# Kernel tuning notes

Hardware: AMD Instinct MI355X
Metric: run time of the kernel (lower is better)

The kernel has to match this reference:

```python
import jax, jax.numpy as jnp
import numpy as np

B, S, D, H = 4, 256, 128, 8
HD = D // H          # head_dim = 16
DD = D // 2          # desc dim = 64 (required: 2*DD == H*HD for edge_type='normal')
T = S + 1            # new_seq (CLS + variables)
NEG_INF = -1e9


def setup_inputs() -> dict:
    key = jax.random.key(0)
    ks = jax.random.split(key, 8)
    p = lambda k, shape: jax.random.normal(k, shape, dtype=jnp.float32) * 0.05
    return {
        "desc_embeddings": jax.random.normal(ks[0], (B, S, DD), dtype=jnp.float32),
        "name_value_embeddings": jax.random.normal(ks[1], (B, T, D), dtype=jnp.float32),
        "Wq": p(ks[2], (D, D)), "bq": jnp.zeros((D,), jnp.float32),
        "Wk": p(ks[3], (D, D)), "bk": jnp.zeros((D,), jnp.float32),
        "Wv": p(ks[4], (D, D)), "bv": jnp.zeros((D,), jnp.float32),
        "aw": p(ks[5], (3 * HD,)),               # attn_proj weight (Linear(3*head_dim, 1))
        "ab": jnp.zeros((), jnp.float32),         # attn_proj bias
    }


def reference(desc_embeddings, name_value_embeddings, Wq, bq, Wk, bk, Wv, bv, aw, ab):
    # Projections -> [B, H, T, HD]
    def proj(W, b):
        y = name_value_embeddings @ W.T + b
        return y.reshape(B, T, H, HD).transpose(0, 2, 1, 3)
    q = proj(Wq, bq)
    k = proj(Wk, bk)
    v = proj(Wv, bv)

    # Structural adjacency: Var-Var without self loops, CLS->Var on, Var->CLS off.
    var_adj = 1.0 - jnp.eye(S, dtype=jnp.float32)          # no_self_loop=True
    adj = jnp.zeros((T, T), jnp.float32)
    adj = adj.at[1:, 1:].set(var_adj).at[0, 1:].set(1.0)   # [T, T], same for all batches

    # Edge attributes: e[b,i,j] = [desc_i, desc_j] on Var-Var block; [desc, desc] on CLS row/col.
    de = desc_embeddings                                    # [B, S, DD]
    edge = jnp.zeros((B, T, T, 2 * DD), jnp.float32)
    edge = edge.at[:, 1:, 1:, :DD].set(de[:, :, None, :])
    edge = edge.at[:, 1:, 1:, DD:].set(de[:, None, :, :])
    cls_e = jnp.concatenate([de, de], axis=-1)              # [B, S, 2*DD]
    edge = edge.at[:, 0, 1:, :].set(cls_e).at[:, 1:, 0, :].set(cls_e)
    eh = edge.reshape(B, T, T, H, HD)                       # per-head edge features

    # attn_proj(cat([q_i, k_j, e_ij])) decomposes linearly (gat_v1: no nonlinearity before):
    # score = q_i.aq + k_j.ak + (adj * e_ij).ae + bias   (edge masked by adjacency pre-linear)
    aq, ak, ae = aw[:HD], aw[HD:2 * HD], aw[2 * HD:]
    sq = jnp.einsum('bhid,d->bhi', q, aq)                   # [B, H, T]
    sk = jnp.einsum('bhjd,d->bhj', k, ak)
    se = jnp.einsum('bijhd,d->bhij', eh, ae) * adj[None, None, :, :]
    logits = sq[:, :, :, None] + sk[:, :, None, :] + se + ab

    # Masked softmax (struct mask as additive -1e9 where adjacency == 0)
    logits = logits + jnp.where(adj == 0.0, NEG_INF, 0.0)[None, None, :, :]
    attn = jax.nn.softmax(logits, axis=-1)                  # [B, H, T, T]; dropout is eval-mode identity

    ctx = jnp.einsum('bhij,bhjd->bhid', attn, v)            # [B, H, T, HD]
    basis_outputs = ctx.transpose(0, 2, 1, 3)               # [B, T, H, HD]
    return basis_outputs, attn
```

## Files before the change

### kernel.cpp

```cpp
#include <hip/hip_runtime.h>

#define NB 4
#define SS 256
#define DM 128
#define NH 8
#define HD 16
#define DDim 64
#define TT 257
#define NPOS (NB*TT)

#define OFF_WQE 0
#define OFF_WKE 1024
#define OFF_BQE 2048
#define OFF_BKE 2064
#define OFF_SQ  2080
#define OFF_SK  10304
#define OFF_G   18528
#define OFF_V   22640

#define ATT_BASE (NB*TT*NH*HD)

__global__ __launch_bounds__(256) void setup_kernel(
    const float* __restrict__ de,
    const float* __restrict__ Wq, const float* __restrict__ bq,
    const float* __restrict__ Wk, const float* __restrict__ bk,
    const float* __restrict__ aw, float* __restrict__ ws)
{
  int tid = threadIdx.x, bid = blockIdx.x;
  if (bid < 4) {
    int idx = bid*256 + tid;
    int h = idx >> 7, e = idx & 127;
    float sq_ = 0.f, sk_ = 0.f;
    #pragma unroll
    for (int d = 0; d < 16; ++d) {
      sq_ += Wq[(h*16+d)*DM + e] * aw[d];
      sk_ += Wk[(h*16+d)*DM + e] * aw[16+d];
    }
    ws[OFF_WQE + idx] = sq_;
    ws[OFF_WKE + idx] = sk_;
    if (bid == 0 && tid < 16) {
      int hh = tid & 7; bool isq = (tid < 8);
      float s = 0.f;
      #pragma unroll
      for (int d = 0; d < 16; ++d)
        s += isq ? bq[hh*16+d]*aw[d] : bk[hh*16+d]*aw[16+d];
      ws[(isq ? OFF_BQE : OFF_BKE) + hh] = s;
    }
  } else {
    int chunk = (bid - 4) * 1028;
    int lim = chunk + 1028;
    for (int r = 0; r < 5; ++r) {
      int gi = chunk + tid + r*256;
      if (gi < lim && gi < 16*TT) {
        int bm = gi / TT, t = gi - bm*TT;
        float val = 0.f;
        if (t > 0) {
          int b = bm >> 2, m = bm & 3;
          const float* dp = de + (b*SS + (t-1))*DDim + m*16;
          #pragma unroll
          for (int d = 0; d < 16; ++d) val += dp[d] * aw[32+d];
        }
        ws[OFF_G + gi] = val;
      }
    }
  }
}

__global__ __launch_bounds__(256) void proj_kernel(
    const float* __restrict__ nve,
    const float* __restrict__ Wv, const float* __restrict__ bv,
    float* __restrict__ ws)
{
  __shared__ float4 xs4[16][32];
  int tid = threadIdx.x;
  int pos0 = blockIdx.x * 16;
  const float4* nve4 = (const float4*)nve;
  for (int idx = tid; idx < 512; idx += 256) {
    int lp = idx >> 5, e4 = idx & 31;
    int pos = pos0 + lp;
    xs4[lp][e4] = (pos < NPOS) ? nve4[pos*32 + e4] : make_float4(0.f,0.f,0.f,0.f);
  }
  __syncthreads();

  int c = tid & 127, ph = tid >> 7;
  const float4* wv4 = (const float4*)(Wv + c*DM);
  bool doe = (c < 16);
  const float4* we4 = doe
      ? (const float4*)(ws + (c < 8 ? OFF_WQE + c*DM : OFF_WKE + (c-8)*DM))
      : wv4;

  float acc[8]  = {0.f,0.f,0.f,0.f,0.f,0.f,0.f,0.f};
  float acce[8] = {0.f,0.f,0.f,0.f,0.f,0.f,0.f,0.f};

  #pragma unroll 4
  for (int e4 = 0; e4 < 32; ++e4) {
    float4 w = wv4[e4];
    #pragma unroll
    for (int p = 0; p < 8; ++p) {
      float4 x = xs4[ph*8+p][e4];
      acc[p] += w.x*x.x + w.y*x.y + w.z*x.z + w.w*x.w;
    }
    if (doe) {
      float4 we = we4[e4];
      #pragma unroll
      for (int p = 0; p < 8; ++p) {
        float4 x = xs4[ph*8+p][e4];
        acce[p] += we.x*x.x + we.y*x.y + we.z*x.z + we.w*x.w;
      }
    }
  }

  int h = c >> 4, d = c & 15;
  float bvc = bv[c];
  float be  = doe ? ws[(c < 8 ? OFF_BQE + c : OFF_BKE + (c-8))] : 0.f;
  for (int p = 0; p < 8; ++p) {
    int pos = pos0 + ph*8 + p;
    if (pos >= NPOS) break;
    int b = pos / TT, t = pos - b*TT;
    ws[OFF_V + ((b*NH + h)*TT + t)*HD + d] = acc[p] + bvc;
    if (c < 8)       ws[OFF_SQ + (b*NH + c)*TT + t]     = acce[p] + be;
    else if (c < 16) ws[OFF_SK + (b*NH + (c-8))*TT + t] = acce[p] + be;
  }
}

__global__ __launch_bounds__(256) void attn_kernel(
    const float* __restrict__ ws, const float* __restrict__ ab_ptr,
    float* __restrict__ out)
{
  __shared__ float p_lds[4][TT+3];
  int tid  = threadIdx.x;
  int wave = tid >> 6, lane = tid & 63;
  int rb = blockIdx.x % 65;
  int bh = blockIdx.x / 65;
  int h = bh & 7, b = bh >> 3;
  int i = rb*4 + wave;
  if (i >= TT) return;

  float ab = ab_ptr[0];
  const float* skp = ws + OFF_SK + bh*TT;
  const float* gp  = ws + OFF_G + (b*4 + (h & 3))*TT;
  const float* vws = ws + OFF_V + bh*TT*HD;

  float Ci = ws[OFF_SQ + bh*TT + i] + ab;
  if (i > 0 && h < 4) Ci += gp[i];
  bool colg = (h >= 4) || (i == 0);

  float l[4];
  float lm = -3.0e38f;
  #pragma unroll
  for (int k = 0; k < 4; ++k) {
    int j = lane + 64*k;
    float u = skp[j] + (colg ? gp[j] : 0.f);
    l[k] = Ci + u;
    bool msk = (j == 0) || (i > 0 && j == i);
    if (!msk) lm = fmaxf(lm, l[k]);
  }
  float l4 = 0.f; bool has4 = false;
  if (lane == 0) {
    l4 = Ci + skp[256] + (colg ? gp[256] : 0.f);
    if (i != 256) { lm = fmaxf(lm, l4); has4 = true; }
  }
  #pragma unroll
  for (int off = 1; off < 64; off <<= 1) lm = fmaxf(lm, __shfl_xor(lm, off));

  float p[4], ps = 0.f;
  #pragma unroll
  for (int k = 0; k < 4; ++k) {
    int j = lane + 64*k;
    bool msk = (j == 0) || (i > 0 && j == i);
    p[k] = msk ? 0.f : expf(l[k] - lm);
    ps += p[k];
  }
  float p4 = has4 ? expf(l4 - lm) : 0.f;
  ps += p4;
  #pragma unroll
  for (int off = 1; off < 64; off <<= 1) ps += __shfl_xor(ps, off);
  float inv = 1.0f / ps;

  float* arow = out + ATT_BASE + (bh*TT + i)*TT;
  #pragma unroll
  for (int k = 0; k < 4; ++k) {
    float v = p[k] * inv;
    arow[lane + 64*k] = v;
    p_lds[wave][lane + 64*k] = v;
  }
  if (lane == 0) { float v = p4 * inv; arow[256] = v; p_lds[wave][256] = v; }

  int g = lane >> 4, d = lane & 15;
  float acc = 0.f;
  #pragma unroll 4
  for (int jj = g; jj < TT; jj += 4)
    acc += p_lds[wave][jj] * vws[jj*HD + d];
  acc += __shfl_xor(acc, 16);
  acc += __shfl_xor(acc, 32);
  if (lane < 16)
    out[((b*TT + i)*NH + h)*HD + lane] = acc;
}

extern "C" void kernel_launch(void* const* d_in, const int* in_sizes, int n_in,
                              void* d_out, int out_size, void* d_ws, size_t ws_size,
                              hipStream_t stream) {
  const float* de  = (const float*)d_in[0];
  const float* nve = (const float*)d_in[1];
  const float* Wq  = (const float*)d_in[2];
  const float* bq  = (const float*)d_in[3];
  const float* Wk  = (const float*)d_in[4];
  const float* bk  = (const float*)d_in[5];
  const float* Wv  = (const float*)d_in[6];
  const float* bv  = (const float*)d_in[7];
  const float* aw  = (const float*)d_in[8];
  const float* ab  = (const float*)d_in[9];
  float* out = (float*)d_out;
  float* ws  = (float*)d_ws;

  setup_kernel<<<8, 256, 0, stream>>>(de, Wq, bq, Wk, bk, aw, ws);
  proj_kernel<<<(NPOS + 15)/16, 256, 0, stream>>>(nve, Wv, bv, ws);
  attn_kernel<<<32*65, 256, 0, stream>>>(ws, ab, out);
}
```

Measured before the change: 35.27 us.

## Merge setup into projection kernel and stage V/scores in LDS for attention

Removes the separate setup kernel by folding the q/k score reductions and edge-score precomputation into the projection kernel. The projection now computes full q and k rows and reduces them against the attention weights with wave shuffles, using smaller blocks (4 positions) and many more of them. The attention kernel loads V, key scores and edge scores for a (batch, head) into LDS once and handles 8 rows per block instead of 4, and it switches to fast __expf. This cuts one launch and repeated global reads of V, at the cost of more FLOPs in the projection and a larger LDS footprint per attention block.

New measurement: 40.01 us. 13.4% more time.

```diff
diff --git a/kernel.cpp b/kernel.cpp
--- a/kernel.cpp
+++ b/kernel.cpp
@@ -9,117 +9,78 @@
 #define TT 257
 #define NPOS (NB*TT)
 
-#define OFF_WQE 0
-#define OFF_WKE 1024
-#define OFF_BQE 2048
-#define OFF_BKE 2064
 #define OFF_SQ  2080
 #define OFF_SK  10304
 #define OFF_G   18528
 #define OFF_V   22640
-
 #define ATT_BASE (NB*TT*NH*HD)
 
-__global__ __launch_bounds__(256) void setup_kernel(
-    const float* __restrict__ de,
+__global__ __launch_bounds__(256) void proj_kernel(
+    const float* __restrict__ de, const float* __restrict__ nve,
     const float* __restrict__ Wq, const float* __restrict__ bq,
     const float* __restrict__ Wk, const float* __restrict__ bk,
+    const float* __restrict__ Wv, const float* __restrict__ bv,
     const float* __restrict__ aw, float* __restrict__ ws)
 {
-  int tid = threadIdx.x, bid = blockIdx.x;
-  if (bid < 4) {
-    int idx = bid*256 + tid;
-    int h = idx >> 7, e = idx & 127;
-    float sq_ = 0.f, sk_ = 0.f;
-    #pragma unroll
-    for (int d = 0; d < 16; ++d) {
-      sq_ += Wq[(h*16+d)*DM + e] * aw[d];
-      sk_ += Wk[(h*16+d)*DM + e] * aw[16+d];
-    }
-    ws[OFF_WQE + idx] = sq_;
-    ws[OFF_WKE + idx] = sk_;
-    if (bid == 0 && tid < 16) {
-      int hh = tid & 7; bool isq = (tid < 8);
-      float s = 0.f;
-      #pragma unroll
-      for (int d = 0; d < 16; ++d)
-        s += isq ? bq[hh*16+d]*aw[d] : bk[hh*16+d]*aw[16+d];
-      ws[(isq ? OFF_BQE : OFF_BKE) + hh] = s;
-    }
-  } else {
-    int chunk = (bid - 4) * 1028;
-    int lim = chunk + 1028;
-    for (int r = 0; r < 5; ++r) {
-      int gi = chunk + tid + r*256;
-      if (gi < lim && gi < 16*TT) {
-        int bm = gi / TT, t = gi - bm*TT;
-        float val = 0.f;
-        if (t > 0) {
-          int b = bm >> 2, m = bm & 3;
-          const float* dp = de + (b*SS + (t-1))*DDim + m*16;
-          #pragma unroll
-          for (int d = 0; d < 16; ++d) val += dp[d] * aw[32+d];
-        }
-        ws[OFF_G + gi] = val;
-      }
-    }
-  }
-}
-
-__global__ __launch_bounds__(256) void proj_kernel(
-    const float* __restrict__ nve,
-    const float* __restrict__ Wv, const float* __restrict__ bv,
-    float* __restrict__ ws)
-{
-  __shared__ float4 xs4[16][32];
+  __shared__ float4 xs4[4][32];
   int tid = threadIdx.x;
-  int pos0 = blockIdx.x * 16;
-  const float4* nve4 = (const float4*)nve;
-  for (int idx = tid; idx < 512; idx += 256) {
-    int lp = idx >> 5, e4 = idx & 31;
-    int pos = pos0 + lp;
-    xs4[lp][e4] = (pos < NPOS) ? nve4[pos*32 + e4] : make_float4(0.f,0.f,0.f,0.f);
+  int pos0 = blockIdx.x * 4;
+  if (tid < 128) {
+    int lp = tid >> 5, e4 = tid & 31;
+    xs4[lp][e4] = ((const float4*)nve)[(pos0 + lp)*32 + e4];
   }
   __syncthreads();
 
   int c = tid & 127, ph = tid >> 7;
+  int dd = c & 15, h = c >> 4;
+  const float4* wq4 = (const float4*)(Wq + c*DM);
+  const float4* wk4 = (const float4*)(Wk + c*DM);
   const float4* wv4 = (const float4*)(Wv + c*DM);
-  bool doe = (c < 16);
-  const float4* we4 = doe
-      ? (const float4*)(ws + (c < 8 ? OFF_WQE + c*DM : OFF_WKE + (c-8)*DM))
-      : wv4;
+  float aqd = aw[dd], akd = aw[16 + dd];
 
-  float acc[8]  = {0.f,0.f,0.f,0.f,0.f,0.f,0.f,0.f};
-  float acce[8] = {0.f,0.f,0.f,0.f,0.f,0.f,0.f,0.f};
+  float accq[2] = {bq[c], bq[c]};
+  float acck[2] = {bk[c], bk[c]};
+  float accv[2] = {bv[c], bv[c]};
 
   #pragma unroll 4
   for (int e4 = 0; e4 < 32; ++e4) {
-    float4 w = wv4[e4];
+    float4 wq = wq4[e4], wk = wk4[e4], wv = wv4[e4];
     #pragma unroll
-    for (int p = 0; p < 8; ++p) {
-      float4 x = xs4[ph*8+p][e4];
-      acc[p] += w.x*x.x + w.y*x.y + w.z*x.z + w.w*x.w;
-    }
-    if (doe) {
-      float4 we = we4[e4];
-      #pragma unroll
-      for (int p = 0; p < 8; ++p) {
-        float4 x = xs4[ph*8+p][e4];
-        acce[p] += we.x*x.x + we.y*x.y + we.z*x.z + we.w*x.w;
-      }
+    for (int p = 0; p < 2; ++p) {
+      float4 x = xs4[ph*2 + p][e4];
+      accq[p] += wq.x*x.x + wq.y*x.y + wq.z*x.z + wq.w*x.w;
+      acck[p] += wk.x*x.x + wk.y*x.y + wk.z*x.z + wk.w*x.w;
+      accv[p] += wv.x*x.x + wv.y*x.y + wv.z*x.z + wv.w*x.w;
     }
   }
 
-  int h = c >> 4, d = c & 15;
-  float bvc = bv[c];
-  float be  = doe ? ws[(c < 8 ? OFF_BQE + c : OFF_BKE + (c-8))] : 0.f;
-  for (int p = 0; p < 8; ++p) {
-    int pos = pos0 + ph*8 + p;
-    if (pos >= NPOS) break;
+  #pragma unroll
+  for (int p = 0; p < 2; ++p) {
+    int pos = pos0 + ph*2 + p;
     int b = pos / TT, t = pos - b*TT;
-    ws[OFF_V + ((b*NH + h)*TT + t)*HD + d] = acc[p] + bvc;
-    if (c < 8)       ws[OFF_SQ + (b*NH + c)*TT + t]     = acce[p] + be;
-    else if (c < 16) ws[OFF_SK + (b*NH + (c-8))*TT + t] = acce[p] + be;
+    ws[OFF_V + ((b*NH + h)*TT + t)*HD + dd] = accv[p];
+    float vq = accq[p] * aqd, vk = acck[p] * akd;
+    vq += __shfl_xor(vq, 1); vq += __shfl_xor(vq, 2);
+    vq += __shfl_xor(vq, 4); vq += __shfl_xor(vq, 8);
+    vk += __shfl_xor(vk, 1); vk += __shfl_xor(vk, 2);
+    vk += __shfl_xor(vk, 4); vk += __shfl_xor(vk, 8);
+    if (dd == 0) {
+      ws[OFF_SQ + (b*NH + h)*TT + t] = vq;
+      ws[OFF_SK + (b*NH + h)*TT + t] = vk;
+    }
+  }
+
+  if (tid < 16) {
+    int gi = blockIdx.x * 16 + tid;
+    int bm = gi / TT, t = gi - bm*TT;
+    float val = 0.f;
+    if (t > 0) {
+      int b = bm >> 2, m = bm & 3;
+      const float* dp = de + (b*SS + (t-1))*DDim + m*16;
+      #pragma unroll
+      for (int d = 0; d < 16; ++d) val += dp[d] * aw[32 + d];
+    }
+    ws[OFF_G + gi] = val;
   }
 }
 
@@ -127,74 +88,94 @@
     const float* __restrict__ ws, const float* __restrict__ ab_ptr,
     float* __restrict__ out)
 {
-  __shared__ float p_lds[4][TT+3];
+  __shared__ float4 v_lds4[TT*4];
+  __shared__ float u_lds[TT+3];
+  __shared__ float g_lds[TT+3];
+  __shared__ float p_lds[4][260];
+  const float* v_lds = (const float*)v_lds4;
+
   int tid  = threadIdx.x;
   int wave = tid >> 6, lane = tid & 63;
-  int rb = blockIdx.x % 65;
-  int bh = blockIdx.x / 65;
+  int rb = blockIdx.x % 33;
+  int bh = blockIdx.x / 33;
   int h = bh & 7, b = bh >> 3;
-  int i = rb*4 + wave;
-  if (i >= TT) return;
+  float ab = ab_ptr[0];
 
-  float ab = ab_ptr[0];
-  const float* skp = ws + OFF_SK + bh*TT;
-  const float* gp  = ws + OFF_G + (b*4 + (h & 3))*TT;
-  const float* vws = ws + OFF_V + bh*TT*HD;
+  const float4* v4  = (const float4*)(ws + OFF_V + bh*TT*HD);
+  const float* skp  = ws + OFF_SK + bh*TT;
+  const float* gp   = ws + OFF_G + (b*4 + (h & 3))*TT;
 
-  float Ci = ws[OFF_SQ + bh*TT + i] + ab;
-  if (i > 0 && h < 4) Ci += gp[i];
-  bool colg = (h >= 4) || (i == 0);
+  #pragma unroll
+  for (int r = 0; r < 5; ++r) {
+    int idx = tid + r*256;
+    if (idx < TT*4) v_lds4[idx] = v4[idx];
+  }
+  for (int j = tid; j < TT; j += 256) { u_lds[j] = skp[j]; g_lds[j] = gp[j]; }
+  __syncthreads();
 
-  float l[4];
-  float lm = -3.0e38f;
-  #pragma unroll
-  for (int k = 0; k < 4; ++k) {
-    int j = lane + 64*k;
-    float u = skp[j] + (colg ? gp[j] : 0.f);
-    l[k] = Ci + u;
-    bool msk = (j == 0) || (i > 0 && j == i);
-    if (!msk) lm = fmaxf(lm, l[k]);
+  bool hlo = (h < 4);
+  for (int rr = 0; rr < 2; ++rr) {
+    int i = rb*8 + rr*4 + wave;
+    if (i >= TT) break;
+
+    float Ci = ws[OFF_SQ + bh*TT + i] + ab;
+    if (i > 0 && hlo) Ci += g_lds[i];
+    bool colg = (!hlo) || (i == 0);
+
+    float l[4];
+    float lm = -3.0e38f;
+    #pragma unroll
+    for (int k = 0; k < 4; ++k) {
+      int j = lane + 64*k;
+      float u = u_lds[j] + (colg ? g_lds[j] : 0.f);
+      l[k] = Ci + u;
+      bool msk = (j == 0) || (i > 0 && j == i);
+      if (!msk) lm = fmaxf(lm, l[k]);
+    }
+    float l4 = 0.f; bool has4 = false;
+    if (lane == 0) {
+      l4 = Ci + u_lds[256] + (colg ? g_lds[256] : 0.f);
+      if (i != 256) { lm = fmaxf(lm, l4); has4 = true; }
+    }
+    #pragma unroll
+    for (int off = 1; off < 64; off <<= 1) lm = fmaxf(lm, __shfl_xor(lm, off));
+
+    float p[4], ps = 0.f;
+    #pragma unroll
+    for (int k = 0; k < 4; ++k) {
+      int j = lane + 64*k;
+      bool msk = (j == 0) || (i > 0 && j == i);
+      p[k] = msk ? 0.f : __expf(l[k] - lm);
+      ps += p[k];
+    }
+    float p4 = has4 ? __expf(l4 - lm) : 0.f;
+    ps += p4;
+    #pragma unroll
+    for (int off = 1; off < 64; off <<= 1) ps += __shfl_xor(ps, off);
+    float inv = 1.0f / ps;
+
+    float* arow = out + ATT_BASE + (bh*TT + i)*TT;
+    #pragma unroll
+    for (int k = 0; k < 4; ++k) {
+      float v = p[k] * inv;
+      arow[lane + 64*k] = v;
+      p_lds[wave][lane + 64*k] = v;
+    }
+    if (lane == 0) { float v = p4 * inv; arow[256] = v; p_lds[wave][256] = v; }
+
+    int g = lane >> 4, d = lane & 15;
+    float acc = 0.f;
+    #pragma unroll 8
+    for (int it = 0; it < 64; ++it) {
+      int jj = g + 4*it;
+      acc += p_lds[wave][jj] * v_lds[jj*HD + d];
+    }
+    if (g == 0) acc += p_lds[wave][256] * v_lds[256*HD + d];
+    acc += __shfl_xor(acc, 16);
+    acc += __shfl_xor(acc, 32);
+    if (lane < 16)
+      out[((b*TT + i)*NH + h)*HD + lane] = acc;
   }
-  float l4 = 0.f; bool has4 = false;
-  if (lane == 0) {
-    l4 = Ci + skp[256] + (colg ? gp[256] : 0.f);
-    if (i != 256) { lm = fmaxf(lm, l4); has4 = true; }
-  }
-  #pragma unroll
-  for (int off = 1; off < 64; off <<= 1) lm = fmaxf(lm, __shfl_xor(lm, off));
-
-  float p[4], ps = 0.f;
-  #pragma unroll
-  for (int k = 0; k < 4; ++k) {
-    int j = lane + 64*k;
-    bool msk = (j == 0) || (i > 0 && j == i);
-    p[k] = msk ? 0.f : expf(l[k] - lm);
-    ps += p[k];
-  }
-  float p4 = has4 ? expf(l4 - lm) : 0.f;
-  ps += p4;
-  #pragma unroll
-  for (int off = 1; off < 64; off <<= 1) ps += __shfl_xor(ps, off);
-  float inv = 1.0f / ps;
-
-  float* arow = out + ATT_BASE + (bh*TT + i)*TT;
-  #pragma unroll
-  for (int k = 0; k < 4; ++k) {
-    float v = p[k] * inv;
-    arow[lane + 64*k] = v;
-    p_lds[wave][lane + 64*k] = v;
-  }
-  if (lane == 0) { float v = p4 * inv; arow[256] = v; p_lds[wave][256] = v; }
-
-  int g = lane >> 4, d = lane & 15;
-  float acc = 0.f;
-  #pragma unroll 4
-  for (int jj = g; jj < TT; jj += 4)
-    acc += p_lds[wave][jj] * vws[jj*HD + d];
-  acc += __shfl_xor(acc, 16);
-  acc += __shfl_xor(acc, 32);
-  if (lane < 16)
-    out[((b*TT + i)*NH + h)*HD + lane] = acc;
 }
 
 extern "C" void kernel_launch(void* const* d_in, const int* in_sizes, int n_in,
@@ -213,7 +194,6 @@
   float* out = (float*)d_out;
   float* ws  = (float*)d_ws;
 
-  setup_kernel<<<8, 256, 0, stream>>>(de, Wq, bq, Wk, bk, aw, ws);
-  proj_kernel<<<(NPOS + 15)/16, 256, 0, stream>>>(nve, Wv, bv, ws);
-  attn_kernel<<<32*65, 256, 0, stream>>>(ws, ab, out);
+  proj_kernel<<<NPOS/4, 256, 0, stream>>>(de, nve, Wq, bq, Wk, bk, Wv, bv, aw, ws);
+  attn_kernel<<<32*33, 256, 0, stream>>>(ws, ab, out);
 }
```
